# Optimization experiments

Measured on AMD Instinct MI355X. Metric: run time of the kernel, lower is better.

## Reference

```python
import jax, jax.numpy as jnp
import numpy as np

# Grid constants from init_kwargs: output_shape = [1, 10, 200, 176, 64]
D, H, W, C = 10, 200, 176, 64
N_VOX = 30000


def _conv_block(x, w, scale, bias, stride, pad):
    # x: [N,C,D,H,W]; w: [O,I,kd,kh,kw]; ZeroPad3d then valid Conv3d,
    # then fused (inference) BatchNorm3d + ReLU.
    x = jnp.pad(x, ((0, 0), (0, 0), (pad[0], pad[0]), (pad[1], pad[1]), (pad[2], pad[2])))
    x = jax.lax.conv_general_dilated(
        x, w, window_strides=stride, padding='VALID',
        dimension_numbers=('NCDHW', 'OIDHW', 'NCDHW'))
    s = scale[None, :, None, None, None]
    b = bias[None, :, None, None, None]
    return jax.nn.relu(x * s + b)


def setup_inputs() -> dict:
    key = jax.random.key(0)
    kf, kd, kh, kw, k1, k2, k3, ks = jax.random.split(key, 8)
    voxel_features = jax.random.normal(kf, (N_VOX, C), dtype=jnp.float32)
    # coors columns: (batch_idx, d, h, w) each in range
    b_idx = jnp.zeros((N_VOX,), dtype=jnp.int32)  # batch_size = 1
    d_idx = jax.random.randint(kd, (N_VOX,), 0, D, dtype=jnp.int32)
    h_idx = jax.random.randint(kh, (N_VOX,), 0, H, dtype=jnp.int32)
    w_idx = jax.random.randint(kw, (N_VOX,), 0, W, dtype=jnp.int32)
    coors = jnp.stack([b_idx, d_idx, h_idx, w_idx], axis=1)
    fan = 1.0 / np.sqrt(C * 27)
    W1 = jax.random.normal(k1, (64, C, 3, 3, 3), dtype=jnp.float32) * fan
    W2 = jax.random.normal(k2, (64, 64, 3, 3, 3), dtype=jnp.float32) * fan
    W3 = jax.random.normal(k3, (64, 64, 3, 3, 3), dtype=jnp.float32) * fan
    ks1, ks2, ks3 = jax.random.split(ks, 3)
    scale1 = jax.random.uniform(ks1, (64,), dtype=jnp.float32, minval=0.5, maxval=1.5)
    scale2 = jax.random.uniform(ks2, (64,), dtype=jnp.float32, minval=0.5, maxval=1.5)
    scale3 = jax.random.uniform(ks3, (64,), dtype=jnp.float32, minval=0.5, maxval=1.5)
    bias1 = jax.random.normal(jax.random.fold_in(ks1, 1), (64,), dtype=jnp.float32) * 0.1
    bias2 = jax.random.normal(jax.random.fold_in(ks2, 1), (64,), dtype=jnp.float32) * 0.1
    bias3 = jax.random.normal(jax.random.fold_in(ks3, 1), (64,), dtype=jnp.float32) * 0.1
    return {
        'voxel_features': voxel_features, 'coors': coors, 'batch_size': 1,
        'W1': W1, 'scale1': scale1, 'bias1': bias1,
        'W2': W2, 'scale2': scale2, 'bias2': bias2,
        'W3': W3, 'scale3': scale3, 'bias3': bias3,
    }


def reference(voxel_features, coors, batch_size,
              W1, scale1, bias1, W2, scale2, bias2, W3, scale3, bias3):
    # scatter_nd: sparse voxel features -> dense [B, D, H, W, C]
    dense = jnp.zeros((batch_size, D, H, W, C), dtype=voxel_features.dtype)
    dense = dense.at[coors[:, 0], coors[:, 1], coors[:, 2], coors[:, 3]].set(voxel_features)
    x = dense.transpose(0, 4, 1, 2, 3)  # [B, C, D, H, W]
    # middle_conv: Pad(1)+Conv3d s=(2,1,1); Pad(0,1,1)+Conv3d s=1; Pad(1)+Conv3d s=(2,1,1)
    x = _conv_block(x, W1, scale1, bias1, (2, 1, 1), (1, 1, 1))   # D: 10 -> 5
    x = _conv_block(x, W2, scale2, bias2, (1, 1, 1), (0, 1, 1))   # D: 5 -> 3
    x = _conv_block(x, W3, scale3, bias3, (2, 1, 1), (1, 1, 1))   # D: 3 -> 2
    N, Cc, Dd, Hh, Ww = x.shape
    return x.reshape(N, Cc * Dd, Hh, Ww)  # [B, 128, H, W]
```

## Files before the change

kernel.cpp:

```cpp
#include <hip/hip_runtime.h>
#include <cstddef>

#define HH 200
#define WW 176
#define HP 202
#define WP 178
#define D_IN 10
#define D1 5
#define D2 3
#define D3 2
#define SLICE ((size_t)HP * WP * 64)

#define LA_BYTES 64512
#define LB_BYTES 8192
#define LDS_TOTAL (LA_BYTES + 2 * LB_BYTES)

typedef _Float16 h8 __attribute__((ext_vector_type(8)));
typedef float f4 __attribute__((ext_vector_type(4)));

__device__ __forceinline__ void gl_lds16(const void* g, void* l) {
    __builtin_amdgcn_global_load_lds(
        (const __attribute__((address_space(1))) void*)g,
        (__attribute__((address_space(3))) void*)l, 16, 0, 0);
}

__global__ __launch_bounds__(256) void prep_k(const float* __restrict__ W1,
                                              const float* __restrict__ W2,
                                              const float* __restrict__ W3,
                                              _Float16* __restrict__ wdst,
                                              _Float16* __restrict__ A2,
                                              _Float16* __restrict__ A3,
                                              const int* __restrict__ coors,
                                              int* __restrict__ winner, int nvox) {
    const int b = blockIdx.x;
    if (b < 8) {
        _Float16* base = (b < D1) ? (A2 + (size_t)b * SLICE) : (A3 + (size_t)(b - D1) * SLICE);
        const h8 z = {};
        for (int t = threadIdx.x; t < 6080; t += 256) {
            size_t off;
            if (t < 2848) {
                int r = t / 1424, c = t - r * 1424;
                off = (size_t)(r ? (HP - 1) : 0) * WP * 64 + (size_t)c * 8;
            } else {
                int u = t - 2848;
                int c = u / 1616, v = u - c * 1616;
                int hr = v >> 3, o = v & 7;
                off = ((size_t)hr * WP + (c ? (WP - 1) : 0)) * 64 + (size_t)o * 8;
            }
            *(h8*)(base + off) = z;
        }
    } else if (b < 8 + 1296) {
        int idx = (b - 8) * 256 + threadIdx.x;
        if (idx < 3 * 27 * 64 * 64) {
            int set = idx / 110592;
            int r = idx - set * 110592;
            const float* src = set == 0 ? W1 : (set == 1 ? W2 : W3);
            int ci = r & 63;
            int co = (r >> 6) & 63;
            int tap = r >> 12;
            int s = ci >> 3, j = ci & 7;
            wdst[set * 110592 + tap * 4096 + co * 64 + (((s ^ (co & 7)) << 3) | j)] =
                (_Float16)src[(co * 64 + ci) * 27 + tap];
        }
    } else {
        int v = (b - 1304) * 256 + threadIdx.x;
        if (v < nvox) {
            int d = coors[v * 4 + 1], h = coors[v * 4 + 2], w = coors[v * 4 + 3];
            atomicMax(&winner[(d * HH + h) * WW + w], v + 1);
        }
    }
}

__global__ __launch_bounds__(256) void scatter_k(const float* __restrict__ feat,
                                                 const int* __restrict__ coors,
                                                 const int* __restrict__ winner,
                                                 _Float16* __restrict__ A, int nvox) {
    int v = blockIdx.x * 4 + (threadIdx.x >> 6);
    int ci = threadIdx.x & 63;
    if (v >= nvox) return;
    int d = coors[v * 4 + 1], h = coors[v * 4 + 2], w = coors[v * 4 + 3];
    if (winner[(d * HH + h) * WW + w] != v + 1) return;
    int P = w + 1;
    int swz = (((ci >> 3) ^ (P & 7)) << 3) | (ci & 7);
    A[(size_t)d * SLICE + ((size_t)(h + 1) * WP + P) * 64 + swz] = (_Float16)feat[v * 64 + ci];
}

template <int FINAL>
__global__ __launch_bounds__(512, 4) void conv_mfma_k(
    const _Float16* __restrict__ in, void* __restrict__ outp,
    const _Float16* __restrict__ wt,
    const float* __restrict__ scale, const float* __restrict__ bias,
    int inD, int strideD, int padD) {
    __shared__ char smem_raw[LDS_TOTAL];
    _Float16* la = (_Float16*)smem_raw;
    char* lb0 = smem_raw + LA_BYTES;
    char* lb1 = smem_raw + LA_BYTES + LB_BYTES;

    const int lane = threadIdx.x & 63;
    const int wave = threadIdx.x >> 6;
    const int l16 = lane & 15;
    const int quad = lane >> 4;
    const int h0 = blockIdx.y * 8;
    const int wb = blockIdx.x * 48;
    const int d = blockIdx.z;

    int kd_lo = padD - d * strideD; if (kd_lo < 0) kd_lo = 0;
    int kd_hi = inD - 1 - d * strideD + padD; if (kd_hi > 2) kd_hi = 2;

    f4 acc[3][4];
#pragma unroll
    for (int mt = 0; mt < 3; ++mt)
#pragma unroll
        for (int nt = 0; nt < 4; ++nt) acc[mt][nt] = (f4){0.f, 0.f, 0.f, 0.f};

    for (int kd = kd_lo; kd <= kd_hi; ++kd) {
        const int zd = d * strideD + kd - padD;
        const _Float16* __restrict__ aplane = in + (size_t)zd * SLICE;
        const _Float16* __restrict__ wkd = wt + (size_t)kd * 9 * 4096;

        for (int j = wave; j < 63; j += 8) {
            int c = j * 64 + lane;
            if (c > 3999) c = 3999;
            int r = c / 400;
            int rem = c - r * 400;
            int px = rem >> 3, s = rem & 7;
            int g = wb + px; if (g > 177) g = 177;
            gl_lds16(aplane + ((size_t)(h0 + r) * WP + g) * 64 + s * 8,
                     smem_raw + j * 1024);
        }
        gl_lds16(wkd + (size_t)(wave * 64 + lane) * 8, lb0 + wave * 1024);

#pragma unroll
        for (int t = 0; t < 9; ++t) {
            const int kh = t / 3;
            const int kw = t - 3 * kh;
            char* lbc = (t & 1) ? lb1 : lb0;

            if (t < 8) {
                char* lbn = (t & 1) ? lb0 : lb1;
                gl_lds16(wkd + (size_t)(t + 1) * 4096 + (size_t)(wave * 64 + lane) * 8,
                         lbn + wave * 1024);
                asm volatile("s_waitcnt vmcnt(1)" ::: "memory");
            } else {
                asm volatile("s_waitcnt vmcnt(0)" ::: "memory");
            }
            __builtin_amdgcn_sched_barrier(0);
            __builtin_amdgcn_s_barrier();
            __builtin_amdgcn_sched_barrier(0);

            const _Float16* lb = (const _Float16*)lbc;
#pragma unroll
            for (int ch = 0; ch < 2; ++ch) {
                const int q = ch * 4 + quad;
                h8 b[4];
#pragma unroll
                for (int nt = 0; nt < 4; ++nt)
                    b[nt] = *(const h8*)(lb + (nt * 16 + l16) * 64 +
                                         ((q ^ (l16 & 7)) << 3));
#pragma unroll
                for (int mt = 0; mt < 3; ++mt) {
                    const int px = mt * 16 + l16 + kw;
                    h8 a = *(const h8*)(la + ((size_t)(wave + kh) * 50 + px) * 64 +
                                        ((q ^ (px & 7)) << 3));
#pragma unroll
                    for (int nt = 0; nt < 4; ++nt)
                        acc[mt][nt] = __builtin_amdgcn_mfma_f32_16x16x32_f16(
                            a, b[nt], acc[mt][nt], 0, 0, 0);
                }
            }
            asm volatile("s_waitcnt lgkmcnt(0)" ::: "memory");
            __builtin_amdgcn_sched_barrier(0);
            __builtin_amdgcn_s_barrier();
            __builtin_amdgcn_sched_barrier(0);
        }
    }

    const int h = h0 + wave;
    if (FINAL) {
#pragma unroll
        for (int nt = 0; nt < 4; ++nt) {
            const int co = nt * 16 + l16;
            const float s = scale[co];
            const float bb = bias[co];
#pragma unroll
            for (int mt = 0; mt < 3; ++mt) {
                const int w0 = wb + mt * 16 + quad * 4;
                if (w0 < WW) {
                    f4 v;
#pragma unroll
                    for (int r = 0; r < 4; ++r) {
                        float x = acc[mt][nt][r] * s + bb;
                        v[r] = x > 0.f ? x : 0.f;
                    }
                    *(f4*)((float*)outp + (((size_t)(co * 2 + d)) * HH + h) * WW + w0) = v;
                }
            }
        }
    } else {
        _Float16* ep = (_Float16*)smem_raw + (size_t)wave * (48 * 72);
#pragma unroll
        for (int nt = 0; nt < 4; ++nt) {
            const int co = nt * 16 + l16;
            const float s = scale[co];
            const float bb = bias[co];
#pragma unroll
            for (int mt = 0; mt < 3; ++mt) {
#pragma unroll
                for (int r = 0; r < 4; ++r) {
                    float x = acc[mt][nt][r] * s + bb;
                    x = x > 0.f ? x : 0.f;
                    ep[(mt * 16 + quad * 4 + r) * 72 + co] = (_Float16)x;
                }
            }
        }
        const int lim = (WW - wb) * 8;
#pragma unroll
        for (int cv = 0; cv < 6; ++cv) {
            if (cv * 64 < lim) {
                const int c2 = cv * 64 + lane;
                const int pxl = c2 >> 3, s = c2 & 7;
                h8 v = *(const h8*)(ep + pxl * 72 + s * 8);
                const int P = wb + pxl + 1;
                *(h8*)((_Float16*)outp + (size_t)d * SLICE +
                       ((size_t)(h + 1) * WP + P) * 64 + ((s ^ (P & 7)) << 3)) = v;
            }
        }
    }
}

extern "C" void kernel_launch(void* const* d_in, const int* in_sizes, int n_in,
                              void* d_out, int out_size, void* d_ws, size_t ws_size,
                              hipStream_t stream) {
    const float* feat   = (const float*)d_in[0];
    const int*   coors  = (const int*)d_in[1];
    const float* W1     = (const float*)d_in[3];
    const float* scale1 = (const float*)d_in[4];
    const float* bias1  = (const float*)d_in[5];
    const float* W2     = (const float*)d_in[6];
    const float* scale2 = (const float*)d_in[7];
    const float* bias2  = (const float*)d_in[8];
    const float* W3     = (const float*)d_in[9];
    const float* scale3 = (const float*)d_in[10];
    const float* bias3  = (const float*)d_in[11];
    const int nvox = in_sizes[0] / 64;

    const size_t nA1 = (size_t)D_IN * SLICE;
    const size_t nWin = (size_t)D_IN * HH * WW;
    const size_t nA2 = (size_t)D1 * SLICE;
    const size_t nA3 = (size_t)D2 * SLICE;
    const size_t nWT = (size_t)27 * 64 * 64;

    _Float16* A1 = (_Float16*)d_ws;
    int* win = (int*)(A1 + nA1);
    _Float16* A2 = (_Float16*)(win + nWin);
    _Float16* A3 = A2 + nA2;
    _Float16* wt1 = A3 + nA3;
    _Float16* wt2 = wt1 + nWT;
    _Float16* wt3 = wt2 + nWT;

    hipMemsetAsync(d_ws, 0, nA1 * sizeof(_Float16) + nWin * sizeof(int), stream);

    const int win_blk = (nvox + 255) / 256;
    prep_k<<<8 + 1296 + win_blk, 256, 0, stream>>>(W1, W2, W3, wt1, A2, A3,
                                                   coors, win, nvox);
    scatter_k<<<(nvox + 3) / 4, 256, 0, stream>>>(feat, coors, win, A1, nvox);

    dim3 blk(512);
    conv_mfma_k<0><<<dim3(4, 25, D1), blk, 0, stream>>>(A1, A2, wt1, scale1, bias1, D_IN, 2, 1);
    conv_mfma_k<0><<<dim3(4, 25, D2), blk, 0, stream>>>(A2, A3, wt2, scale2, bias2, D1, 1, 0);
    conv_mfma_k<1><<<dim3(4, 25, D3), blk, 0, stream>>>(A3, (float*)d_out, wt3, scale3, bias3, D2, 2, 1);
}
```

Before: 201.9 us.

## Prefetch next depth plane via registers and shrink conv2/conv3 blocks to 4 waves

The activation tile for the next kd plane is now loaded into registers during the last tap of the current plane and written to LDS afterwards. The weights for the next plane are double-buffered across the plane boundary. This hides the global-load latency that previously stalled each kd iteration. Conv2 and conv3 now use 4-wave blocks (twice the grid) to raise block count for their small depth, and setprio raises priority around the MFMA section. Smaller blocks re-read more halo rows, and the register staging adds pressure.

```diff
diff --git a/kernel.cpp b/kernel.cpp
--- a/kernel.cpp
+++ b/kernel.cpp
@@ -10,10 +10,6 @@
 #define D2 3
 #define D3 2
 #define SLICE ((size_t)HP * WP * 64)
-
-#define LA_BYTES 64512
-#define LB_BYTES 8192
-#define LDS_TOTAL (LA_BYTES + 2 * LB_BYTES)
 
 typedef _Float16 h8 __attribute__((ext_vector_type(8)));
 typedef float f4 __attribute__((ext_vector_type(4)));
@@ -85,62 +81,110 @@
     A[(size_t)d * SLICE + ((size_t)(h + 1) * WP + P) * 64 + swz] = (_Float16)feat[v * 64 + ci];
 }
 
-template <int FINAL>
-__global__ __launch_bounds__(512, 4) void conv_mfma_k(
+template <int FINAL, int NW>
+__global__ __launch_bounds__(NW * 64, (NW == 8 ? 4 : 2)) void conv_mfma_k(
     const _Float16* __restrict__ in, void* __restrict__ outp,
     const _Float16* __restrict__ wt,
     const float* __restrict__ scale, const float* __restrict__ bias,
     int inD, int strideD, int padD) {
-    __shared__ char smem_raw[LDS_TOTAL];
+    constexpr int ROWS_A = NW + 2;
+    constexpr int NSTG = (ROWS_A * 400 + 63) / 64;
+    constexpr int LA = NSTG * 1024;
+    constexpr int APW = (NSTG + NW - 1) / NW;
+    constexpr int BI = 8 / NW;
+    constexpr int CMAX = ROWS_A * 400 - 1;
+
+    __shared__ char smem_raw[LA + 2 * 8192];
     _Float16* la = (_Float16*)smem_raw;
-    char* lb0 = smem_raw + LA_BYTES;
-    char* lb1 = smem_raw + LA_BYTES + LB_BYTES;
+    char* lb0 = smem_raw + LA;
+    char* lb1 = smem_raw + LA + 8192;
 
     const int lane = threadIdx.x & 63;
     const int wave = threadIdx.x >> 6;
     const int l16 = lane & 15;
     const int quad = lane >> 4;
-    const int h0 = blockIdx.y * 8;
+    const int h0 = blockIdx.y * NW;
     const int wb = blockIdx.x * 48;
     const int d = blockIdx.z;
 
     int kd_lo = padD - d * strideD; if (kd_lo < 0) kd_lo = 0;
     int kd_hi = inD - 1 - d * strideD + padD; if (kd_hi > 2) kd_hi = 2;
 
+    uint4 areg[APW];
+    auto issue_a = [&](const _Float16* aplane) {
+#pragma unroll
+        for (int i = 0; i < APW; ++i) {
+            int j = wave + i * NW;
+            if (j < NSTG) {
+                int c = j * 64 + lane;
+                if (c > CMAX) c = CMAX;
+                int r = c / 400;
+                int rem = c - r * 400;
+                int px = rem >> 3, s = rem & 7;
+                int g = wb + px; if (g > 177) g = 177;
+                areg[i] = *(const uint4*)(aplane +
+                              ((size_t)(h0 + r) * WP + g) * 64 + s * 8);
+            }
+        }
+    };
+    auto commit_a = [&]() {
+#pragma unroll
+        for (int i = 0; i < APW; ++i) {
+            int j = wave + i * NW;
+            if (j < NSTG)
+                *(uint4*)(smem_raw + j * 1024 + (size_t)lane * 16) = areg[i];
+        }
+    };
+    auto stage_b = [&](const _Float16* wsrc, char* lbW) {
+#pragma unroll
+        for (int i = 0; i < BI; ++i) {
+            int k = i * NW + wave;
+            gl_lds16(wsrc + (size_t)(k * 64 + lane) * 8, lbW + k * 1024);
+        }
+    };
+
     f4 acc[3][4];
 #pragma unroll
     for (int mt = 0; mt < 3; ++mt)
 #pragma unroll
         for (int nt = 0; nt < 4; ++nt) acc[mt][nt] = (f4){0.f, 0.f, 0.f, 0.f};
+
+    issue_a(in + (size_t)(d * strideD + kd_lo - padD) * SLICE);
+    stage_b(wt + (size_t)kd_lo * 9 * 4096, lb0);
+    int base = 0;
 
     for (int kd = kd_lo; kd <= kd_hi; ++kd) {
         const int zd = d * strideD + kd - padD;
-        const _Float16* __restrict__ aplane = in + (size_t)zd * SLICE;
         const _Float16* __restrict__ wkd = wt + (size_t)kd * 9 * 4096;
 
-        for (int j = wave; j < 63; j += 8) {
-            int c = j * 64 + lane;
-            if (c > 3999) c = 3999;
-            int r = c / 400;
-            int rem = c - r * 400;
-            int px = rem >> 3, s = rem & 7;
-            int g = wb + px; if (g > 177) g = 177;
-            gl_lds16(aplane + ((size_t)(h0 + r) * WP + g) * 64 + s * 8,
-                     smem_raw + j * 1024);
-        }
-        gl_lds16(wkd + (size_t)(wave * 64 + lane) * 8, lb0 + wave * 1024);
+        asm volatile("s_waitcnt vmcnt(0)" ::: "memory");
+        __builtin_amdgcn_sched_barrier(0);
+        commit_a();
+        asm volatile("s_waitcnt lgkmcnt(0)" ::: "memory");
+        __builtin_amdgcn_sched_barrier(0);
+        __builtin_amdgcn_s_barrier();
+        __builtin_amdgcn_sched_barrier(0);
 
 #pragma unroll
         for (int t = 0; t < 9; ++t) {
             const int kh = t / 3;
             const int kw = t - 3 * kh;
-            char* lbc = (t & 1) ? lb1 : lb0;
+            const int pr = (t & 1) ^ base;
+            char* lbR = pr ? lb1 : lb0;
+            char* lbW = pr ? lb0 : lb1;
 
             if (t < 8) {
-                char* lbn = (t & 1) ? lb0 : lb1;
-                gl_lds16(wkd + (size_t)(t + 1) * 4096 + (size_t)(wave * 64 + lane) * 8,
-                         lbn + wave * 1024);
-                asm volatile("s_waitcnt vmcnt(1)" ::: "memory");
+                stage_b(wkd + (t + 1) * 4096, lbW);
+                if constexpr (BI == 1)
+                    asm volatile("s_waitcnt vmcnt(1)" ::: "memory");
+                else
+                    asm volatile("s_waitcnt vmcnt(2)" ::: "memory");
+            } else if (kd < kd_hi) {
+                stage_b(wkd + 9 * 4096, lbW);
+                if constexpr (BI == 1)
+                    asm volatile("s_waitcnt vmcnt(1)" ::: "memory");
+                else
+                    asm volatile("s_waitcnt vmcnt(2)" ::: "memory");
             } else {
                 asm volatile("s_waitcnt vmcnt(0)" ::: "memory");
             }
@@ -148,7 +192,11 @@
             __builtin_amdgcn_s_barrier();
             __builtin_amdgcn_sched_barrier(0);
 
-            const _Float16* lb = (const _Float16*)lbc;
+            if (t == 8 && kd < kd_hi)
+                issue_a(in + (size_t)(zd + 1) * SLICE);
+
+            const _Float16* lb = (const _Float16*)lbR;
+            __builtin_amdgcn_s_setprio(1);
 #pragma unroll
             for (int ch = 0; ch < 2; ++ch) {
                 const int q = ch * 4 + quad;
@@ -168,11 +216,13 @@
                             a, b[nt], acc[mt][nt], 0, 0, 0);
                 }
             }
+            __builtin_amdgcn_s_setprio(0);
             asm volatile("s_waitcnt lgkmcnt(0)" ::: "memory");
             __builtin_amdgcn_sched_barrier(0);
             __builtin_amdgcn_s_barrier();
             __builtin_amdgcn_sched_barrier(0);
         }
+        base ^= 1;
     }
 
     const int h = h0 + wave;
@@ -265,8 +315,7 @@
                                                    coors, win, nvox);
     scatter_k<<<(nvox + 3) / 4, 256, 0, stream>>>(feat, coors, win, A1, nvox);
 
-    dim3 blk(512);
-    conv_mfma_k<0><<<dim3(4, 25, D1), blk, 0, stream>>>(A1, A2, wt1, scale1, bias1, D_IN, 2, 1);
-    conv_mfma_k<0><<<dim3(4, 25, D2), blk, 0, stream>>>(A2, A3, wt2, scale2, bias2, D1, 1, 0);
-    conv_mfma_k<1><<<dim3(4, 25, D3), blk, 0, stream>>>(A3, (float*)d_out, wt3, scale3, bias3, D2, 2, 1);
-}
+    conv_mfma_k<0, 8><<<dim3(4, 25, D1), 512, 0, stream>>>(A1, A2, wt1, scale1, bias1, D_IN, 2, 1);
+    conv_mfma_k<0, 4><<<dim3(4, 50, D2), 256, 0, stream>>>(A2, A3, wt2, scale2, bias2, D1, 1, 0);
+    conv_mfma_k<1, 4><<<dim3(4, 50, D3), 256, 0, stream>>>(A3, (float*)d_out, wt3, scale3, bias3, D2, 2, 1);
+}
```

Measured after the change: 266.1 us. +31.8%, slower.

## Halve waves per conv block so each wave computes two output rows

Applied to the files above, without the earlier changes.

The conv kernel now runs 256 threads (4 waves) per block instead of 512. Each wave accumulates two output rows, so every B-fragment loaded from LDS feeds twice as many MFMAs. Loads of the input tile and weight slices are spread over the fewer waves. s_setprio is raised around the MFMA section. The cost is twice the accumulator registers per wave and fewer waves to hide latency, with launch bounds changed to (256,2).

```diff
diff --git a/kernel.cpp b/kernel.cpp
--- a/kernel.cpp
+++ b/kernel.cpp
@@ -86,7 +86,7 @@
 }
 
 template <int FINAL>
-__global__ __launch_bounds__(512, 4) void conv_mfma_k(
+__global__ __launch_bounds__(256, 2) void conv_mfma_k(
     const _Float16* __restrict__ in, void* __restrict__ outp,
     const _Float16* __restrict__ wt,
     const float* __restrict__ scale, const float* __restrict__ bias,
@@ -107,18 +107,20 @@
     int kd_lo = padD - d * strideD; if (kd_lo < 0) kd_lo = 0;
     int kd_hi = inD - 1 - d * strideD + padD; if (kd_hi > 2) kd_hi = 2;
 
-    f4 acc[3][4];
-#pragma unroll
-    for (int mt = 0; mt < 3; ++mt)
-#pragma unroll
-        for (int nt = 0; nt < 4; ++nt) acc[mt][nt] = (f4){0.f, 0.f, 0.f, 0.f};
+    f4 acc[2][3][4];
+#pragma unroll
+    for (int rr = 0; rr < 2; ++rr)
+#pragma unroll
+        for (int mt = 0; mt < 3; ++mt)
+#pragma unroll
+            for (int nt = 0; nt < 4; ++nt) acc[rr][mt][nt] = (f4){0.f, 0.f, 0.f, 0.f};
 
     for (int kd = kd_lo; kd <= kd_hi; ++kd) {
         const int zd = d * strideD + kd - padD;
         const _Float16* __restrict__ aplane = in + (size_t)zd * SLICE;
         const _Float16* __restrict__ wkd = wt + (size_t)kd * 9 * 4096;
 
-        for (int j = wave; j < 63; j += 8) {
+        for (int j = wave; j < 63; j += 4) {
             int c = j * 64 + lane;
             if (c > 3999) c = 3999;
             int r = c / 400;
@@ -128,7 +130,11 @@
             gl_lds16(aplane + ((size_t)(h0 + r) * WP + g) * 64 + s * 8,
                      smem_raw + j * 1024);
         }
-        gl_lds16(wkd + (size_t)(wave * 64 + lane) * 8, lb0 + wave * 1024);
+#pragma unroll
+        for (int i = 0; i < 2; ++i) {
+            int k = i * 4 + wave;
+            gl_lds16(wkd + (size_t)(k * 64 + lane) * 8, lb0 + k * 1024);
+        }
 
 #pragma unroll
         for (int t = 0; t < 9; ++t) {
@@ -138,9 +144,13 @@
 
             if (t < 8) {
                 char* lbn = (t & 1) ? lb0 : lb1;
-                gl_lds16(wkd + (size_t)(t + 1) * 4096 + (size_t)(wave * 64 + lane) * 8,
-                         lbn + wave * 1024);
-                asm volatile("s_waitcnt vmcnt(1)" ::: "memory");
+#pragma unroll
+                for (int i = 0; i < 2; ++i) {
+                    int k = i * 4 + wave;
+                    gl_lds16(wkd + (size_t)(t + 1) * 4096 + (size_t)(k * 64 + lane) * 8,
+                             lbn + k * 1024);
+                }
+                asm volatile("s_waitcnt vmcnt(2)" ::: "memory");
             } else {
                 asm volatile("s_waitcnt vmcnt(0)" ::: "memory");
             }
@@ -149,6 +159,7 @@
             __builtin_amdgcn_sched_barrier(0);
 
             const _Float16* lb = (const _Float16*)lbc;
+            __builtin_amdgcn_s_setprio(1);
 #pragma unroll
             for (int ch = 0; ch < 2; ++ch) {
                 const int q = ch * 4 + quad;
@@ -158,16 +169,21 @@
                     b[nt] = *(const h8*)(lb + (nt * 16 + l16) * 64 +
                                          ((q ^ (l16 & 7)) << 3));
 #pragma unroll
-                for (int mt = 0; mt < 3; ++mt) {
-                    const int px = mt * 16 + l16 + kw;
-                    h8 a = *(const h8*)(la + ((size_t)(wave + kh) * 50 + px) * 64 +
-                                        ((q ^ (px & 7)) << 3));
-#pragma unroll
-                    for (int nt = 0; nt < 4; ++nt)
-                        acc[mt][nt] = __builtin_amdgcn_mfma_f32_16x16x32_f16(
-                            a, b[nt], acc[mt][nt], 0, 0, 0);
-                }
-            }
+                for (int rr = 0; rr < 2; ++rr) {
+                    const int row = wave * 2 + rr + kh;
+#pragma unroll
+                    for (int mt = 0; mt < 3; ++mt) {
+                        const int px = mt * 16 + l16 + kw;
+                        h8 a = *(const h8*)(la + ((size_t)row * 50 + px) * 64 +
+                                            ((q ^ (px & 7)) << 3));
+#pragma unroll
+                        for (int nt = 0; nt < 4; ++nt)
+                            acc[rr][mt][nt] = __builtin_amdgcn_mfma_f32_16x16x32_f16(
+                                a, b[nt], acc[rr][mt][nt], 0, 0, 0);
+                    }
+                }
+            }
+            __builtin_amdgcn_s_setprio(0);
             asm volatile("s_waitcnt lgkmcnt(0)" ::: "memory");
             __builtin_amdgcn_sched_barrier(0);
             __builtin_amdgcn_s_barrier();
@@ -175,7 +191,6 @@
         }
     }
 
-    const int h = h0 + wave;
     if (FINAL) {
 #pragma unroll
         for (int nt = 0; nt < 4; ++nt) {
@@ -183,46 +198,59 @@
             const float s = scale[co];
             const float bb = bias[co];
 #pragma unroll
-            for (int mt = 0; mt < 3; ++mt) {
-                const int w0 = wb + mt * 16 + quad * 4;
-                if (w0 < WW) {
-                    f4 v;
-#pragma unroll
-                    for (int r = 0; r < 4; ++r) {
-                        float x = acc[mt][nt][r] * s + bb;
-                        v[r] = x > 0.f ? x : 0.f;
+            for (int rr = 0; rr < 2; ++rr) {
+                const int h = h0 + wave * 2 + rr;
+#pragma unroll
+                for (int mt = 0; mt < 3; ++mt) {
+                    const int w0 = wb + mt * 16 + quad * 4;
+                    if (w0 < WW) {
+                        f4 v;
+#pragma unroll
+                        for (int r = 0; r < 4; ++r) {
+                            float x = acc[rr][mt][nt][r] * s + bb;
+                            v[r] = x > 0.f ? x : 0.f;
+                        }
+                        *(f4*)((float*)outp + (((size_t)(co * 2 + d)) * HH + h) * WW + w0) = v;
                     }
-                    *(f4*)((float*)outp + (((size_t)(co * 2 + d)) * HH + h) * WW + w0) = v;
                 }
             }
         }
     } else {
-        _Float16* ep = (_Float16*)smem_raw + (size_t)wave * (48 * 72);
+        _Float16* epb = (_Float16*)smem_raw;
 #pragma unroll
         for (int nt = 0; nt < 4; ++nt) {
             const int co = nt * 16 + l16;
             const float s = scale[co];
             const float bb = bias[co];
 #pragma unroll
-            for (int mt = 0; mt < 3; ++mt) {
-#pragma unroll
-                for (int r = 0; r < 4; ++r) {
-                    float x = acc[mt][nt][r] * s + bb;
-                    x = x > 0.f ? x : 0.f;
-                    ep[(mt * 16 + quad * 4 + r) * 72 + co] = (_Float16)x;
+            for (int rr = 0; rr < 2; ++rr) {
+                _Float16* ep = epb + (size_t)(wave * 2 + rr) * (48 * 72);
+#pragma unroll
+                for (int mt = 0; mt < 3; ++mt) {
+#pragma unroll
+                    for (int r = 0; r < 4; ++r) {
+                        float x = acc[rr][mt][nt][r] * s + bb;
+                        x = x > 0.f ? x : 0.f;
+                        ep[(mt * 16 + quad * 4 + r) * 72 + co] = (_Float16)x;
+                    }
                 }
             }
         }
         const int lim = (WW - wb) * 8;
 #pragma unroll
-        for (int cv = 0; cv < 6; ++cv) {
-            if (cv * 64 < lim) {
-                const int c2 = cv * 64 + lane;
-                const int pxl = c2 >> 3, s = c2 & 7;
-                h8 v = *(const h8*)(ep + pxl * 72 + s * 8);
-                const int P = wb + pxl + 1;
-                *(h8*)((_Float16*)outp + (size_t)d * SLICE +
-                       ((size_t)(h + 1) * WP + P) * 64 + ((s ^ (P & 7)) << 3)) = v;
+        for (int rr = 0; rr < 2; ++rr) {
+            const int h = h0 + wave * 2 + rr;
+            const _Float16* ep = epb + (size_t)(wave * 2 + rr) * (48 * 72);
+#pragma unroll
+            for (int cv = 0; cv < 6; ++cv) {
+                if (cv * 64 < lim) {
+                    const int c2 = cv * 64 + lane;
+                    const int pxl = c2 >> 3, s = c2 & 7;
+                    h8 v = *(const h8*)(ep + pxl * 72 + s * 8);
+                    const int P = wb + pxl + 1;
+                    *(h8*)((_Float16*)outp + (size_t)d * SLICE +
+                           ((size_t)(h + 1) * WP + P) * 64 + ((s ^ (P & 7)) << 3)) = v;
+                }
             }
         }
     }
@@ -265,7 +293,7 @@
                                                    coors, win, nvox);
     scatter_k<<<(nvox + 3) / 4, 256, 0, stream>>>(feat, coors, win, A1, nvox);
 
-    dim3 blk(512);
+    dim3 blk(256);
     conv_mfma_k<0><<<dim3(4, 25, D1), blk, 0, stream>>>(A1, A2, wt1, scale1, bias1, D_IN, 2, 1);
     conv_mfma_k<0><<<dim3(4, 25, D2), blk, 0, stream>>>(A2, A3, wt2, scale2, bias2, D1, 1, 0);
     conv_mfma_k<1><<<dim3(4, 25, D3), blk, 0, stream>>>(A3, (float*)d_out, wt3, scale3, bias3, D2, 2, 1);
```

After: 189.9 us. 1.06x faster.

## Double-buffer input plane in LDS to prefetch next depth slice during MFMA

Applied to the files above, without the earlier changes.

The input activation tile now gets two LDS buffers. The next kd plane is loaded in slices interleaved with the nine kh/kw taps, and the first weight tap of the next kd is prefetched at the end of the current one. This hides the global-to-LDS load stall that previously sat at the start of each kd iteration. It also raises MFMA wave priority with s_setprio. In exchange LDS use roughly doubles and launch bounds drop from 4 to 2 blocks per CU, which cuts occupancy.

```diff
diff --git a/kernel.cpp b/kernel.cpp
--- a/kernel.cpp
+++ b/kernel.cpp
@@ -13,7 +13,7 @@
 
 #define LA_BYTES 64512
 #define LB_BYTES 8192
-#define LDS_TOTAL (LA_BYTES + 2 * LB_BYTES)
+#define LDS_TOTAL (2 * LA_BYTES + 2 * LB_BYTES)
 
 typedef _Float16 h8 __attribute__((ext_vector_type(8)));
 typedef float f4 __attribute__((ext_vector_type(4)));
@@ -86,15 +86,14 @@
 }
 
 template <int FINAL>
-__global__ __launch_bounds__(512, 4) void conv_mfma_k(
+__global__ __launch_bounds__(512, 2) void conv_mfma_k(
     const _Float16* __restrict__ in, void* __restrict__ outp,
     const _Float16* __restrict__ wt,
     const float* __restrict__ scale, const float* __restrict__ bias,
     int inD, int strideD, int padD) {
     __shared__ char smem_raw[LDS_TOTAL];
-    _Float16* la = (_Float16*)smem_raw;
-    char* lb0 = smem_raw + LA_BYTES;
-    char* lb1 = smem_raw + LA_BYTES + LB_BYTES;
+    char* lb0 = smem_raw + 2 * LA_BYTES;
+    char* lb1 = lb0 + LB_BYTES;
 
     const int lane = threadIdx.x & 63;
     const int wave = threadIdx.x >> 6;
@@ -107,39 +106,65 @@
     int kd_lo = padD - d * strideD; if (kd_lo < 0) kd_lo = 0;
     int kd_hi = inD - 1 - d * strideD + padD; if (kd_hi > 2) kd_hi = 2;
 
+    auto stage_a1 = [&](const _Float16* aplane, int j, int abuf) {
+        int c = j * 64 + lane;
+        if (c > 3999) c = 3999;
+        int r = c / 400;
+        int rem = c - r * 400;
+        int px = rem >> 3, s = rem & 7;
+        int g = wb + px; if (g > 177) g = 177;
+        gl_lds16(aplane + ((size_t)(h0 + r) * WP + g) * 64 + s * 8,
+                 smem_raw + abuf * LA_BYTES + j * 1024);
+    };
+
     f4 acc[3][4];
 #pragma unroll
     for (int mt = 0; mt < 3; ++mt)
 #pragma unroll
         for (int nt = 0; nt < 4; ++nt) acc[mt][nt] = (f4){0.f, 0.f, 0.f, 0.f};
+
+    int ab = 0;
+    int base = 0;
+
+    {
+        const _Float16* ap = in + (size_t)(d * strideD + kd_lo - padD) * SLICE;
+#pragma unroll
+        for (int i = 0; i < 8; ++i) {
+            int j = i * 8 + wave; if (j > 62) j = 62;
+            stage_a1(ap, j, 0);
+        }
+        gl_lds16(wt + (size_t)kd_lo * 9 * 4096 + (size_t)(wave * 64 + lane) * 8,
+                 lb0 + wave * 1024);
+    }
 
     for (int kd = kd_lo; kd <= kd_hi; ++kd) {
         const int zd = d * strideD + kd - padD;
-        const _Float16* __restrict__ aplane = in + (size_t)zd * SLICE;
         const _Float16* __restrict__ wkd = wt + (size_t)kd * 9 * 4096;
-
-        for (int j = wave; j < 63; j += 8) {
-            int c = j * 64 + lane;
-            if (c > 3999) c = 3999;
-            int r = c / 400;
-            int rem = c - r * 400;
-            int px = rem >> 3, s = rem & 7;
-            int g = wb + px; if (g > 177) g = 177;
-            gl_lds16(aplane + ((size_t)(h0 + r) * WP + g) * 64 + s * 8,
-                     smem_raw + j * 1024);
-        }
-        gl_lds16(wkd + (size_t)(wave * 64 + lane) * 8, lb0 + wave * 1024);
+        const _Float16* __restrict__ anext = in + (size_t)(zd + 1) * SLICE;
+        const _Float16* la = (const _Float16*)(smem_raw + ab * LA_BYTES);
 
 #pragma unroll
         for (int t = 0; t < 9; ++t) {
             const int kh = t / 3;
             const int kw = t - 3 * kh;
-            char* lbc = (t & 1) ? lb1 : lb0;
+            const int pr = (t & 1) ^ base;
+            char* lbR = pr ? lb1 : lb0;
+            char* lbW = pr ? lb0 : lb1;
 
             if (t < 8) {
-                char* lbn = (t & 1) ? lb0 : lb1;
+                if (kd < kd_hi) {
+                    int j = t * 8 + wave; if (j > 62) j = 62;
+                    stage_a1(anext, j, ab ^ 1);
+                }
                 gl_lds16(wkd + (size_t)(t + 1) * 4096 + (size_t)(wave * 64 + lane) * 8,
-                         lbn + wave * 1024);
+                         lbW + wave * 1024);
+                if (kd < kd_hi)
+                    asm volatile("s_waitcnt vmcnt(2)" ::: "memory");
+                else
+                    asm volatile("s_waitcnt vmcnt(1)" ::: "memory");
+            } else if (kd < kd_hi) {
+                gl_lds16(wkd + (size_t)9 * 4096 + (size_t)(wave * 64 + lane) * 8,
+                         lbW + wave * 1024);
                 asm volatile("s_waitcnt vmcnt(1)" ::: "memory");
             } else {
                 asm volatile("s_waitcnt vmcnt(0)" ::: "memory");
@@ -148,7 +173,8 @@
             __builtin_amdgcn_s_barrier();
             __builtin_amdgcn_sched_barrier(0);
 
-            const _Float16* lb = (const _Float16*)lbc;
+            const _Float16* lb = (const _Float16*)lbR;
+            __builtin_amdgcn_s_setprio(1);
 #pragma unroll
             for (int ch = 0; ch < 2; ++ch) {
                 const int q = ch * 4 + quad;
@@ -168,11 +194,14 @@
                             a, b[nt], acc[mt][nt], 0, 0, 0);
                 }
             }
+            __builtin_amdgcn_s_setprio(0);
             asm volatile("s_waitcnt lgkmcnt(0)" ::: "memory");
             __builtin_amdgcn_sched_barrier(0);
             __builtin_amdgcn_s_barrier();
             __builtin_amdgcn_sched_barrier(0);
         }
+        ab ^= 1;
+        base ^= 1;
     }
 
     const int h = h0 + wave;
```

Result: no change. 199.5 us (-1.2%).
